# Optimization experiments

Hardware: AMD Instinct MI355X
Metric: run time of the kernel (lower is better)

The kernel has to match this reference:

```python
import jax, jax.numpy as jnp
import numpy as np

NUM_USERS, NUM_ITEMS, NUM_GROUPS = 100000, 50000, 20000
D = 64
B, M = 16384, 50


def setup_inputs() -> dict:
    key = jax.random.key(0)
    ks = jax.random.split(key, 16)
    inp = {
        "group_inputs": jax.random.randint(ks[0], (B,), 0, NUM_GROUPS),
        "item_inputs": jax.random.randint(ks[1], (B,), 0, NUM_ITEMS),
        "member_ids": jax.random.randint(ks[2], (B, M), 0, NUM_USERS),
        "member_lengths": jax.random.randint(ks[3], (B,), 0, M),
        # embedding tables (xavier-ish scale)
        "user_table": jax.random.normal(ks[4], (NUM_USERS, D), jnp.float32) * 0.05,
        "item_table": jax.random.normal(ks[5], (NUM_ITEMS, D), jnp.float32) * 0.05,
        "group_table": jax.random.normal(ks[6], (NUM_GROUPS, D), jnp.float32) * 0.05,
        # attention MLP: 2D -> 16 -> 1
        "att_w1": jax.random.normal(ks[7], (2 * D, 16), jnp.float32) * 0.1,
        "att_b1": jnp.zeros((16,), jnp.float32),
        "att_w2": jax.random.normal(ks[8], (16, 1), jnp.float32) * 0.1,
        "att_b2": jnp.zeros((1,), jnp.float32),
        # predict MLP: 3D -> 8 -> 1
        "pred_w1": jax.random.normal(ks[9], (3 * D, 8), jnp.float32) * 0.1,
        "pred_b1": jnp.zeros((8,), jnp.float32),
        "pred_w2": jax.random.normal(ks[10], (8, 1), jnp.float32) * 0.1,
        "pred_b2": jnp.zeros((1,), jnp.float32),
    }
    return inp


def reference(group_inputs, item_inputs, member_ids, member_lengths,
              user_table, item_table, group_table,
              att_w1, att_b1, att_w2, att_b2,
              pred_w1, pred_b1, pred_w2, pred_b2):
    # mask: at least one valid member per group
    mask = jnp.arange(M)[None, :] <= member_lengths[:, None]          # [B, M] bool
    mem_e = user_table[member_ids]                                    # [B, M, D]
    item_e = item_table[item_inputs]                                  # [B, D]

    # attention over members: concat(member, item) -> 16 -> 1
    gi = jnp.concatenate(
        [mem_e, jnp.broadcast_to(item_e[:, None, :], mem_e.shape)], axis=-1)  # [B, M, 2D]
    h = jax.nn.relu(jnp.einsum('bmk,kh->bmh', gi, att_w1) + att_b1)   # [B, M, 16]
    scores = (jnp.einsum('bmh,ho->bmo', h, att_w2) + att_b2)[..., 0]  # [B, M]
    scores = jnp.where(mask, scores, -jnp.inf)
    at_wt = jax.nn.softmax(scores, axis=-1)                           # [B, M]

    g_att = jnp.einsum('bm,bmd->bd', at_wt, mem_e)                    # [B, D]
    g = g_att + group_table[group_inputs]                             # [B, D]

    elem = g * item_e
    new_e = jnp.concatenate([elem, g, item_e], axis=-1)               # [B, 3D]
    ph = jax.nn.relu(new_e @ pred_w1 + pred_b1)                       # [B, 8]
    y = jax.nn.sigmoid(ph @ pred_w2 + pred_b2)                        # [B, 1]
    return y
```

## Files before the change

### kernel.cpp

```cpp
#include <hip/hip_runtime.h>
#include <math.h>

constexpr int MM = 50;
constexpr int DD = 64;
constexpr int HH = 16;
constexpr int PH = 8;
constexpr int WAVES_PER_BLOCK = 4;

__global__ __launch_bounds__(256) void precompute_kernel(
    const float* __restrict__ user_table,
    const float* __restrict__ item_table,
    const int*   __restrict__ item_inputs,
    const float* __restrict__ att_w1,
    const float* __restrict__ att_b1,
    float* __restrict__ U,
    float* __restrict__ Ib,
    int nU, int B, int userBlocks)
{
    const bool isU = (int)blockIdx.x < userBlocks;
    const float4* rp;
    const float*  w1;
    float* dst;
    float acc[HH];

    if (isU) {
        const int row = (int)blockIdx.x * 256 + (int)threadIdx.x;
        if (row >= nU) return;
        rp  = (const float4*)(user_table + (size_t)row * DD);
        w1  = att_w1;
        dst = U + (size_t)row * HH;
        #pragma unroll
        for (int j = 0; j < HH; ++j) acc[j] = 0.0f;
    } else {
        const int r = ((int)blockIdx.x - userBlocks) * 256 + (int)threadIdx.x;
        if (r >= B) return;
        const int item = item_inputs[r];
        rp  = (const float4*)(item_table + (size_t)item * DD);
        w1  = att_w1 + (size_t)DD * HH;
        dst = Ib + (size_t)r * HH;
        #pragma unroll
        for (int j = 0; j < HH; ++j) acc[j] = att_b1[j];
    }

    #pragma unroll 4
    for (int d4 = 0; d4 < DD / 4; ++d4) {
        const float4 x = rp[d4];
        const float* w = w1 + (size_t)(d4 * 4) * HH;
        #pragma unroll
        for (int j = 0; j < HH; ++j) {
            acc[j] = fmaf(x.x, w[0 * HH + j], acc[j]);
            acc[j] = fmaf(x.y, w[1 * HH + j], acc[j]);
            acc[j] = fmaf(x.z, w[2 * HH + j], acc[j]);
            acc[j] = fmaf(x.w, w[3 * HH + j], acc[j]);
        }
    }

    float4* o4 = (float4*)dst;
    o4[0] = make_float4(acc[0],  acc[1],  acc[2],  acc[3]);
    o4[1] = make_float4(acc[4],  acc[5],  acc[6],  acc[7]);
    o4[2] = make_float4(acc[8],  acc[9],  acc[10], acc[11]);
    o4[3] = make_float4(acc[12], acc[13], acc[14], acc[15]);
}

__global__ __launch_bounds__(256) void agree_main(
    const int* __restrict__ group_inputs,
    const int* __restrict__ item_inputs,
    const int* __restrict__ member_ids,
    const int* __restrict__ member_lengths,
    const float* __restrict__ user_table,
    const float* __restrict__ item_table,
    const float* __restrict__ group_table,
    const float* __restrict__ att_w2,
    const float* __restrict__ att_b2,
    const float* __restrict__ pred_w1,
    const float* __restrict__ pred_b1,
    const float* __restrict__ pred_w2,
    const float* __restrict__ pred_b2,
    const float* __restrict__ U,
    const float* __restrict__ Ib,
    float* __restrict__ out,
    int B)
{
    const int lane = threadIdx.x & 63;
    const int wave = threadIdx.x >> 6;
    const int b = blockIdx.x * WAVES_PER_BLOCK + wave;
    if (b >= B) return;

    const int my_m  = (lane < MM) ? lane : (MM - 1);
    const int my_id = member_ids[b * MM + my_m];
    const int len   = member_lengths[b];

    const float4* up = (const float4*)(U + (size_t)my_id * HH);
    const float4 u0 = up[0], u1 = up[1], u2 = up[2], u3 = up[3];
    const float* ib = Ib + (size_t)b * HH;

    float score = att_b2[0];
    {
        const float uu[HH] = { u0.x,u0.y,u0.z,u0.w, u1.x,u1.y,u1.z,u1.w,
                               u2.x,u2.y,u2.z,u2.w, u3.x,u3.y,u3.z,u3.w };
        #pragma unroll
        for (int j = 0; j < HH; ++j)
            score = fmaf(fmaxf(uu[j] + ib[j], 0.0f), att_w2[j], score);
    }

    const bool valid = (lane < MM) && (lane <= len);
    score = valid ? score : -INFINITY;

    float mx = score;
    #pragma unroll
    for (int off = 32; off > 0; off >>= 1) mx = fmaxf(mx, __shfl_xor(mx, off, 64));
    const float e = valid ? __expf(score - mx) : 0.0f;
    float sum = e;
    #pragma unroll
    for (int off = 32; off > 0; off >>= 1) sum += __shfl_xor(sum, off, 64);
    const float wnorm = e / sum;

    const int d4  = lane & 15;
    const int rep = lane >> 4;
    const int mcnt   = (len < MM - 1 ? len : MM - 1) + 1;
    const int passes = (mcnt + 3) >> 2;

    float4 g4 = make_float4(0.f, 0.f, 0.f, 0.f);
    int pass = 0;
    for (; pass + 2 <= passes; pass += 2) {
        const int m0 = pass * 4 + rep;
        const int m1 = m0 + 4;
        const float w0 = __shfl(wnorm, m0, 64);
        const int   i0 = __shfl(my_id, m0, 64);
        const float w1 = __shfl(wnorm, m1, 64);
        const int   i1 = __shfl(my_id, m1, 64);
        const float4 x0 = ((const float4*)(user_table + (size_t)i0 * DD))[d4];
        const float4 x1 = ((const float4*)(user_table + (size_t)i1 * DD))[d4];
        g4.x = fmaf(w0, x0.x, g4.x); g4.y = fmaf(w0, x0.y, g4.y);
        g4.z = fmaf(w0, x0.z, g4.z); g4.w = fmaf(w0, x0.w, g4.w);
        g4.x = fmaf(w1, x1.x, g4.x); g4.y = fmaf(w1, x1.y, g4.y);
        g4.z = fmaf(w1, x1.z, g4.z); g4.w = fmaf(w1, x1.w, g4.w);
    }
    if (pass < passes) {
        const int m0 = pass * 4 + rep;
        const float w0 = __shfl(wnorm, m0, 64);
        const int   i0 = __shfl(my_id, m0, 64);
        const float4 x0 = ((const float4*)(user_table + (size_t)i0 * DD))[d4];
        g4.x = fmaf(w0, x0.x, g4.x); g4.y = fmaf(w0, x0.y, g4.y);
        g4.z = fmaf(w0, x0.z, g4.z); g4.w = fmaf(w0, x0.w, g4.w);
    }
    #pragma unroll
    for (int off = 16; off <= 32; off <<= 1) {
        g4.x += __shfl_xor(g4.x, off, 64);
        g4.y += __shfl_xor(g4.y, off, 64);
        g4.z += __shfl_xor(g4.z, off, 64);
        g4.w += __shfl_xor(g4.w, off, 64);
    }

    const int gid      = group_inputs[b];
    const int item_idx = item_inputs[b];
    const float4 gr  = ((const float4*)(group_table + (size_t)gid * DD))[d4];
    const float4 it4 = ((const float4*)(item_table + (size_t)item_idx * DD))[d4];
    g4.x += gr.x; g4.y += gr.y; g4.z += gr.z; g4.w += gr.w;
    const float4 e4 = make_float4(g4.x * it4.x, g4.y * it4.y,
                                  g4.z * it4.z, g4.w * it4.w);

    float p[PH];
    #pragma unroll
    for (int j = 0; j < PH; ++j) p[j] = 0.0f;
    {
        const float* wa = pred_w1 + (size_t)(4 * d4) * PH;
        const float* wb = pred_w1 + (size_t)(DD + 4 * d4) * PH;
        const float* wc = pred_w1 + (size_t)(2 * DD + 4 * d4) * PH;
        const float ev[4] = { e4.x, e4.y, e4.z, e4.w };
        const float gv[4] = { g4.x, g4.y, g4.z, g4.w };
        const float iv[4] = { it4.x, it4.y, it4.z, it4.w };
        #pragma unroll
        for (int k = 0; k < 4; ++k) {
            #pragma unroll
            for (int j = 0; j < PH; ++j) {
                p[j] = fmaf(ev[k], wa[k * PH + j],
                       fmaf(gv[k], wb[k * PH + j],
                       fmaf(iv[k], wc[k * PH + j], p[j])));
            }
        }
    }
    #pragma unroll
    for (int off = 1; off <= 8; off <<= 1) {
        #pragma unroll
        for (int j = 0; j < PH; ++j) p[j] += __shfl_xor(p[j], off, 64);
    }

    if (lane == 0) {
        float acc = pred_b2[0];
        #pragma unroll
        for (int j = 0; j < PH; ++j)
            acc = fmaf(fmaxf(p[j] + pred_b1[j], 0.0f), pred_w2[j], acc);
        out[b] = 1.0f / (1.0f + __expf(-acc));
    }
}

__global__ __launch_bounds__(256) void agree_fallback(
    const int* __restrict__ group_inputs,
    const int* __restrict__ item_inputs,
    const int* __restrict__ member_ids,
    const int* __restrict__ member_lengths,
    const float* __restrict__ user_table,
    const float* __restrict__ item_table,
    const float* __restrict__ group_table,
    const float* __restrict__ att_w1,
    const float* __restrict__ att_b1,
    const float* __restrict__ att_w2,
    const float* __restrict__ att_b2,
    const float* __restrict__ pred_w1,
    const float* __restrict__ pred_b1,
    const float* __restrict__ pred_w2,
    const float* __restrict__ pred_b2,
    float* __restrict__ out,
    int B)
{
    __shared__ float lds_wt[WAVES_PER_BLOCK][MM];
    __shared__ int   lds_id[WAVES_PER_BLOCK][MM];

    const int lane = threadIdx.x & 63;
    const int wave = threadIdx.x >> 6;
    const int b = blockIdx.x * WAVES_PER_BLOCK + wave;
    if (b >= B) return;

    const int my_m = (lane < MM) ? lane : (MM - 1);
    const int my_id = member_ids[b * MM + my_m];
    if (lane < MM) lds_id[wave][lane] = my_id;

    const int item_idx = item_inputs[b];
    const float item_d = item_table[(size_t)item_idx * DD + lane];

    float h[HH];
    {
        const float* w1row = att_w1 + (size_t)(DD + lane) * HH;
        #pragma unroll
        for (int j = 0; j < HH; ++j) h[j] = item_d * w1row[j];
        #pragma unroll
        for (int off = 32; off > 0; off >>= 1) {
            #pragma unroll
            for (int j = 0; j < HH; ++j) h[j] += __shfl_xor(h[j], off, 64);
        }
        #pragma unroll
        for (int j = 0; j < HH; ++j) h[j] += att_b1[j];
    }

    const float* myrow = user_table + (size_t)my_id * DD;
    #pragma unroll 4
    for (int d4 = 0; d4 < DD / 4; ++d4) {
        const float4 x = ((const float4*)myrow)[d4];
        const float* w1d = att_w1 + (size_t)(d4 * 4) * HH;
        #pragma unroll
        for (int j = 0; j < HH; ++j) {
            h[j] = fmaf(x.x, w1d[0 * HH + j], h[j]);
            h[j] = fmaf(x.y, w1d[1 * HH + j], h[j]);
            h[j] = fmaf(x.z, w1d[2 * HH + j], h[j]);
            h[j] = fmaf(x.w, w1d[3 * HH + j], h[j]);
        }
    }

    float score = att_b2[0];
    #pragma unroll
    for (int j = 0; j < HH; ++j) score = fmaf(fmaxf(h[j], 0.0f), att_w2[j], score);

    const int len = member_lengths[b];
    const bool valid = (lane < MM) && (lane <= len);
    score = valid ? score : -INFINITY;

    float mx = score;
    #pragma unroll
    for (int off = 32; off > 0; off >>= 1) mx = fmaxf(mx, __shfl_xor(mx, off, 64));
    float e = valid ? __expf(score - mx) : 0.0f;
    float sum = e;
    #pragma unroll
    for (int off = 32; off > 0; off >>= 1) sum += __shfl_xor(sum, off, 64);
    if (lane < MM) lds_wt[wave][lane] = e / sum;
    __builtin_amdgcn_s_waitcnt(0);

    const int mcnt = (len < MM - 1 ? len : MM - 1) + 1;
    float g = 0.0f;
    #pragma unroll 2
    for (int m = 0; m < mcnt; ++m) {
        g = fmaf(lds_wt[wave][m],
                 user_table[(size_t)lds_id[wave][m] * DD + lane], g);
    }
    const int gid = group_inputs[b];
    g += group_table[(size_t)gid * DD + lane];

    const float elem = g * item_d;
    float p[PH];
    {
        const float* pa = pred_w1 + (size_t)lane * PH;
        const float* pb = pred_w1 + (size_t)(DD + lane) * PH;
        const float* pc = pred_w1 + (size_t)(2 * DD + lane) * PH;
        #pragma unroll
        for (int j = 0; j < PH; ++j)
            p[j] = fmaf(elem, pa[j], fmaf(g, pb[j], item_d * pc[j]));
    }
    #pragma unroll
    for (int off = 32; off > 0; off >>= 1) {
        #pragma unroll
        for (int j = 0; j < PH; ++j) p[j] += __shfl_xor(p[j], off, 64);
    }

    if (lane == 0) {
        float acc = pred_b2[0];
        #pragma unroll
        for (int j = 0; j < PH; ++j)
            acc = fmaf(fmaxf(p[j] + pred_b1[j], 0.0f), pred_w2[j], acc);
        out[b] = 1.0f / (1.0f + __expf(-acc));
    }
}

extern "C" void kernel_launch(void* const* d_in, const int* in_sizes, int n_in,
                              void* d_out, int out_size, void* d_ws, size_t ws_size,
                              hipStream_t stream) {
    const int*   group_inputs   = (const int*)d_in[0];
    const int*   item_inputs    = (const int*)d_in[1];
    const int*   member_ids     = (const int*)d_in[2];
    const int*   member_lengths = (const int*)d_in[3];
    const float* user_table     = (const float*)d_in[4];
    const float* item_table     = (const float*)d_in[5];
    const float* group_table    = (const float*)d_in[6];
    const float* att_w1         = (const float*)d_in[7];
    const float* att_b1         = (const float*)d_in[8];
    const float* att_w2         = (const float*)d_in[9];
    const float* att_b2         = (const float*)d_in[10];
    const float* pred_w1        = (const float*)d_in[11];
    const float* pred_b1        = (const float*)d_in[12];
    const float* pred_w2        = (const float*)d_in[13];
    const float* pred_b2        = (const float*)d_in[14];
    float* out = (float*)d_out;

    const int B  = in_sizes[0];
    const int nU = in_sizes[4] / DD;
    const size_t need = ((size_t)nU + (size_t)B) * HH * sizeof(float);
    const int blocks = (B + WAVES_PER_BLOCK - 1) / WAVES_PER_BLOCK;

    if (ws_size >= need) {
        float* U  = (float*)d_ws;
        float* Ib = U + (size_t)nU * HH;
        const int userBlocks = (nU + 255) / 256;
        const int itemBlocks = (B + 255) / 256;
        precompute_kernel<<<userBlocks + itemBlocks, 256, 0, stream>>>(
            user_table, item_table, item_inputs, att_w1, att_b1,
            U, Ib, nU, B, userBlocks);
        agree_main<<<blocks, 256, 0, stream>>>(
            group_inputs, item_inputs, member_ids, member_lengths,
            user_table, item_table, group_table,
            att_w2, att_b2, pred_w1, pred_b1, pred_w2, pred_b2,
            U, Ib, out, B);
    } else {
        agree_fallback<<<blocks, 256, 0, stream>>>(
            group_inputs, item_inputs, member_ids, member_lengths,
            user_table, item_table, group_table,
            att_w1, att_b1, att_w2, att_b2,
            pred_w1, pred_b1, pred_w2, pred_b2,
            out, B);
    }
}
```

Before: 174.7 us.

## Assign one block per batch row and split member gather across waves

```diff
diff --git a/kernel.cpp b/kernel.cpp
--- a/kernel.cpp
+++ b/kernel.cpp
@@ -5,7 +5,6 @@
 constexpr int DD = 64;
 constexpr int HH = 16;
 constexpr int PH = 8;
-constexpr int WAVES_PER_BLOCK = 4;
 
 __global__ __launch_bounds__(256) void precompute_kernel(
     const float* __restrict__ user_table,
@@ -62,7 +61,7 @@
     o4[3] = make_float4(acc[12], acc[13], acc[14], acc[15]);
 }
 
-__global__ __launch_bounds__(256) void agree_main(
+__global__ __launch_bounds__(256) void agree_block(
     const int* __restrict__ group_inputs,
     const int* __restrict__ item_inputs,
     const int* __restrict__ member_ids,
@@ -78,17 +77,19 @@
     const float* __restrict__ pred_b2,
     const float* __restrict__ U,
     const float* __restrict__ Ib,
-    float* __restrict__ out,
-    int B)
+    float* __restrict__ out)
 {
+    __shared__ float lds_part[3][DD];
+
     const int lane = threadIdx.x & 63;
-    const int wave = threadIdx.x >> 6;
-    const int b = blockIdx.x * WAVES_PER_BLOCK + wave;
-    if (b >= B) return;
+    const int wv   = threadIdx.x >> 6;
+    const int b    = blockIdx.x;
 
     const int my_m  = (lane < MM) ? lane : (MM - 1);
     const int my_id = member_ids[b * MM + my_m];
     const int len   = member_lengths[b];
+    const int item_idx = item_inputs[b];
+    const int gid      = group_inputs[b];
 
     const float4* up = (const float4*)(U + (size_t)my_id * HH);
     const float4 u0 = up[0], u1 = up[1], u2 = up[2], u3 = up[3];
@@ -115,73 +116,59 @@
     for (int off = 32; off > 0; off >>= 1) sum += __shfl_xor(sum, off, 64);
     const float wnorm = e / sum;
 
-    const int d4  = lane & 15;
-    const int rep = lane >> 4;
-    const int mcnt   = (len < MM - 1 ? len : MM - 1) + 1;
-    const int passes = (mcnt + 3) >> 2;
-
-    float4 g4 = make_float4(0.f, 0.f, 0.f, 0.f);
-    int pass = 0;
-    for (; pass + 2 <= passes; pass += 2) {
-        const int m0 = pass * 4 + rep;
-        const int m1 = m0 + 4;
-        const float w0 = __shfl(wnorm, m0, 64);
-        const int   i0 = __shfl(my_id, m0, 64);
-        const float w1 = __shfl(wnorm, m1, 64);
-        const int   i1 = __shfl(my_id, m1, 64);
-        const float4 x0 = ((const float4*)(user_table + (size_t)i0 * DD))[d4];
-        const float4 x1 = ((const float4*)(user_table + (size_t)i1 * DD))[d4];
-        g4.x = fmaf(w0, x0.x, g4.x); g4.y = fmaf(w0, x0.y, g4.y);
-        g4.z = fmaf(w0, x0.z, g4.z); g4.w = fmaf(w0, x0.w, g4.w);
-        g4.x = fmaf(w1, x1.x, g4.x); g4.y = fmaf(w1, x1.y, g4.y);
-        g4.z = fmaf(w1, x1.z, g4.z); g4.w = fmaf(w1, x1.w, g4.w);
-    }
-    if (pass < passes) {
-        const int m0 = pass * 4 + rep;
-        const float w0 = __shfl(wnorm, m0, 64);
-        const int   i0 = __shfl(my_id, m0, 64);
-        const float4 x0 = ((const float4*)(user_table + (size_t)i0 * DD))[d4];
-        g4.x = fmaf(w0, x0.x, g4.x); g4.y = fmaf(w0, x0.y, g4.y);
-        g4.z = fmaf(w0, x0.z, g4.z); g4.w = fmaf(w0, x0.w, g4.w);
-    }
-    #pragma unroll
-    for (int off = 16; off <= 32; off <<= 1) {
-        g4.x += __shfl_xor(g4.x, off, 64);
-        g4.y += __shfl_xor(g4.y, off, 64);
-        g4.z += __shfl_xor(g4.z, off, 64);
-        g4.w += __shfl_xor(g4.w, off, 64);
-    }
-
-    const int gid      = group_inputs[b];
-    const int item_idx = item_inputs[b];
-    const float4 gr  = ((const float4*)(group_table + (size_t)gid * DD))[d4];
-    const float4 it4 = ((const float4*)(item_table + (size_t)item_idx * DD))[d4];
-    g4.x += gr.x; g4.y += gr.y; g4.z += gr.z; g4.w += gr.w;
-    const float4 e4 = make_float4(g4.x * it4.x, g4.y * it4.y,
-                                  g4.z * it4.z, g4.w * it4.w);
-
+    const float item_d = item_table[(size_t)item_idx * DD + lane];
+    const float grp_d  = group_table[(size_t)gid * DD + lane];
+
+    const int mcnt = (len < MM - 1 ? len : MM - 1) + 1;
+    float gw = 0.0f;
+    {
+        float w[7]; int id[7]; float x[7];
+        #pragma unroll
+        for (int k = 0; k < 7; ++k) {
+            const int m = wv + 4 * k;
+            w[k]  = __shfl(wnorm, m, 64);
+            id[k] = __shfl(my_id, m, 64);
+        }
+        #pragma unroll
+        for (int k = 0; k < 7; ++k)
+            x[k] = user_table[(size_t)id[k] * DD + lane];
+        #pragma unroll
+        for (int k = 0; k < 7; ++k) gw = fmaf(w[k], x[k], gw);
+    }
+    if (wv + 28 < mcnt) {
+        float w[6]; int id[6]; float x[6];
+        #pragma unroll
+        for (int k = 0; k < 6; ++k) {
+            const int m = wv + 4 * (k + 7);
+            w[k]  = __shfl(wnorm, m, 64);
+            id[k] = __shfl(my_id, m, 64);
+        }
+        #pragma unroll
+        for (int k = 0; k < 6; ++k)
+            x[k] = user_table[(size_t)id[k] * DD + lane];
+        #pragma unroll
+        for (int k = 0; k < 6; ++k) gw = fmaf(w[k], x[k], gw);
+    }
+
+    if (wv) lds_part[wv - 1][lane] = gw;
+    __syncthreads();
+    if (wv) return;
+
+    float g = gw + lds_part[0][lane] + lds_part[1][lane] + lds_part[2][lane];
+    g += grp_d;
+
+    const float elem = g * item_d;
     float p[PH];
-    #pragma unroll
-    for (int j = 0; j < PH; ++j) p[j] = 0.0f;
-    {
-        const float* wa = pred_w1 + (size_t)(4 * d4) * PH;
-        const float* wb = pred_w1 + (size_t)(DD + 4 * d4) * PH;
-        const float* wc = pred_w1 + (size_t)(2 * DD + 4 * d4) * PH;
-        const float ev[4] = { e4.x, e4.y, e4.z, e4.w };
-        const float gv[4] = { g4.x, g4.y, g4.z, g4.w };
-        const float iv[4] = { it4.x, it4.y, it4.z, it4.w };
-        #pragma unroll
-        for (int k = 0; k < 4; ++k) {
-            #pragma unroll
-            for (int j = 0; j < PH; ++j) {
-                p[j] = fmaf(ev[k], wa[k * PH + j],
-                       fmaf(gv[k], wb[k * PH + j],
-                       fmaf(iv[k], wc[k * PH + j], p[j])));
-            }
-        }
-    }
-    #pragma unroll
-    for (int off = 1; off <= 8; off <<= 1) {
+    {
+        const float* pa = pred_w1 + (size_t)lane * PH;
+        const float* pb = pred_w1 + (size_t)(DD + lane) * PH;
+        const float* pc = pred_w1 + (size_t)(2 * DD + lane) * PH;
+        #pragma unroll
+        for (int j = 0; j < PH; ++j)
+            p[j] = fmaf(elem, pa[j], fmaf(g, pb[j], item_d * pc[j]));
+    }
+    #pragma unroll
+    for (int off = 32; off > 0; off >>= 1) {
         #pragma unroll
         for (int j = 0; j < PH; ++j) p[j] += __shfl_xor(p[j], off, 64);
     }
@@ -214,12 +201,12 @@
     float* __restrict__ out,
     int B)
 {
-    __shared__ float lds_wt[WAVES_PER_BLOCK][MM];
-    __shared__ int   lds_id[WAVES_PER_BLOCK][MM];
+    __shared__ float lds_wt[4][MM];
+    __shared__ int   lds_id[4][MM];
 
     const int lane = threadIdx.x & 63;
     const int wave = threadIdx.x >> 6;
-    const int b = blockIdx.x * WAVES_PER_BLOCK + wave;
+    const int b = blockIdx.x * 4 + wave;
     if (b >= B) return;
 
     const int my_m = (lane < MM) ? lane : (MM - 1);
@@ -333,7 +320,6 @@
     const int B  = in_sizes[0];
     const int nU = in_sizes[4] / DD;
     const size_t need = ((size_t)nU + (size_t)B) * HH * sizeof(float);
-    const int blocks = (B + WAVES_PER_BLOCK - 1) / WAVES_PER_BLOCK;
 
     if (ws_size >= need) {
         float* U  = (float*)d_ws;
@@ -343,12 +329,13 @@
         precompute_kernel<<<userBlocks + itemBlocks, 256, 0, stream>>>(
             user_table, item_table, item_inputs, att_w1, att_b1,
             U, Ib, nU, B, userBlocks);
-        agree_main<<<blocks, 256, 0, stream>>>(
+        agree_block<<<B, 256, 0, stream>>>(
             group_inputs, item_inputs, member_ids, member_lengths,
             user_table, item_table, group_table,
             att_w2, att_b2, pred_w1, pred_b1, pred_w2, pred_b2,
-            U, Ib, out, B);
+            U, Ib, out);
     } else {
+        const int blocks = (B + 3) / 4;
         agree_fallback<<<blocks, 256, 0, stream>>>(
             group_inputs, item_inputs, member_ids, member_lengths,
             user_table, item_table, group_table,
```

Result: faster. 150.9 us (-13.6%).
